# Kernel optimization log

Measured on AMD Instinct MI355X. Metric: run time of the kernel, lower is better.

Reference implementation:

```python
import jax, jax.numpy as jnp
import numpy as np

N = 100000
E = 1600000
D_IN = 64
D_HID = 64
D_OUT = 64


def setup_inputs() -> dict:
    key = jax.random.key(0)
    ks = jax.random.split(key, 12)
    x = jax.random.normal(ks[0], (N, D_IN), dtype=jnp.float32)
    edge_index = jax.random.randint(ks[1], (2, E), 0, N, dtype=jnp.int64)
    s1 = 1.0 / np.sqrt(D_IN)
    s2 = 1.0 / np.sqrt(D_HID)
    return {
        "x": x,
        "edge_index": edge_index,
        "W1l": jax.random.uniform(ks[2], (D_HID, D_IN), jnp.float32, -s1, s1),
        "b1l": jax.random.uniform(ks[3], (D_HID,), jnp.float32, -s1, s1),
        "W1r": jax.random.uniform(ks[4], (D_HID, D_IN), jnp.float32, -s1, s1),
        "W2l": jax.random.uniform(ks[5], (D_HID, D_HID), jnp.float32, -s2, s2),
        "b2l": jax.random.uniform(ks[6], (D_HID,), jnp.float32, -s2, s2),
        "W2r": jax.random.uniform(ks[7], (D_HID, D_HID), jnp.float32, -s2, s2),
        "Wout": jax.random.uniform(ks[8], (D_OUT, D_HID), jnp.float32, -s2, s2),
        "bout": jax.random.uniform(ks[9], (D_OUT,), jnp.float32, -s2, s2),
        "drop": 0,
    }


def _sage_conv(x, src, dst, Wl, bl, Wr, n_nodes):
    # PyG SAGEConv, aggr='mean': out = lin_l(mean_j x_j) + lin_r(x_i)
    msg = x[src]                                            # [E, d] gather
    agg = jax.ops.segment_sum(msg, dst, num_segments=n_nodes)
    deg = jax.ops.segment_sum(jnp.ones((src.shape[0],), x.dtype), dst,
                              num_segments=n_nodes)
    mean = agg / jnp.maximum(deg, 1.0)[:, None]             # empty neighborhoods -> 0
    return mean @ Wl.T + bl + x @ Wr.T


def reference(x, edge_index, W1l, b1l, W1r, W2l, b2l, W2r, Wout, bout, drop):
    src, dst = edge_index[0], edge_index[1]
    n = x.shape[0]
    # dropout is identity in eval mode (training=False); drop unused
    h = jax.nn.relu(_sage_conv(x, src, dst, W1l, b1l, W1r, n))
    h = jax.nn.relu(_sage_conv(h, src, dst, W2l, b2l, W2r, n))
    logits = h @ Wout.T + bout
    return jax.nn.log_softmax(logits, axis=1)
```

## Files before the change

kernel.cpp:

```cpp
#include <hip/hip_runtime.h>


#define TB 256
#define TBA 1024
#define NBINA 256
#define XFB 512
#define CAPC 32
#define NBPAD 1024

typedef __attribute__((ext_vector_type(8))) short bf16x8;
typedef __attribute__((ext_vector_type(4))) float f32x4;
typedef __attribute__((ext_vector_type(2))) float f32x2;

__device__ __forceinline__ unsigned short bf16c(float f) {
  union { float f; unsigned u; } v; v.f = f;
  unsigned r = (v.u + 0x7FFFu + ((v.u >> 16) & 1u)) >> 16;
  return (unsigned short)r;
}

__device__ __forceinline__ bf16x8 ld_bf8(const float* p) {
  float4 a = *(const float4*)p;
  float4 b = *(const float4*)(p + 4);
  bf16x8 r;
  r[0] = bf16c(a.x); r[1] = bf16c(a.y); r[2] = bf16c(a.z); r[3] = bf16c(a.w);
  r[4] = bf16c(b.x); r[5] = bf16c(b.y); r[6] = bf16c(b.z); r[7] = bf16c(b.w);
  return r;
}

__device__ __forceinline__ float bflo(unsigned u) { return __uint_as_float(u << 16); }
__device__ __forceinline__ float bfhi(unsigned u) { return __uint_as_float(u & 0xFFFF0000u); }
__device__ __forceinline__ unsigned bfpk(float lo, float hi) {
  return (unsigned)bf16c(lo) | ((unsigned)bf16c(hi) << 16);
}

__global__ __launch_bounds__(1024) void k_binA(
    const int* __restrict__ ei, int E,
    int* __restrict__ cellcnt, unsigned int* __restrict__ bucketData, int NB) {
  __shared__ int lcnt[NBPAD];
  __shared__ int s_nz;
  if (threadIdx.x == 0) s_nz = 0;
  for (int i = threadIdx.x; i < NBPAD; i += TBA) lcnt[i] = 0;
  __syncthreads();
  int nz = 0;
  for (int i = threadIdx.x; i < 2048; i += TBA) nz |= ei[2 * i + 1];
  if (nz) atomicOr(&s_nz, 1);
  __syncthreads();
  bool m64 = (s_nz == 0);
  int bb = blockIdx.x;

  long long e0 = (long long)E * bb / NBINA;
  long long e1 = (long long)E * (bb + 1) / NBINA;
  for (long long e = e0 + threadIdx.x; e < e1; e += TBA) {
    int src, dst;
    if (m64) {
      src = ((const int2*)ei)[e].x;
      dst = ((const int2*)ei)[(long long)E + e].x;
    } else {
      src = ei[e];
      dst = ei[(long long)E + e];
    }
    int b = dst >> 7;
    int pos = atomicAdd(&lcnt[b], 1);
    if (pos < CAPC)
      bucketData[((size_t)b * NBINA + bb) * CAPC + pos] =
          ((unsigned)(dst & 127) << 24) | (unsigned)src;
  }
  __syncthreads();
  for (int b = threadIdx.x; b < NB; b += TBA) cellcnt[bb * NBPAD + b] = lcnt[b];
}

__global__ __launch_bounds__(256) void k_binB_xf(
    const unsigned int* __restrict__ bucketData, const int* __restrict__ cellcnt,
    int* __restrict__ colp, int* __restrict__ cnt, int NB,
    const float* __restrict__ xin, const float* __restrict__ Wl,
    const float* __restrict__ Wr, const float* __restrict__ bl,
    unsigned short* __restrict__ y, unsigned short* __restrict__ zout, int n) {
  if (blockIdx.x < (unsigned)NB) {
    __shared__ unsigned int slice[128 * 64];
    __shared__ int lcnt[128];
    int b = blockIdx.x;
    for (int i = threadIdx.x; i < 128; i += TB) lcnt[i] = 0;
    __syncthreads();
    int c = cellcnt[threadIdx.x * NBPAD + b];
    if (c > CAPC) c = CAPC;
    const unsigned int* cell = bucketData + ((size_t)b * NBINA + threadIdx.x) * CAPC;
    for (int k = 0; k < c; ++k) {
      unsigned int rec = cell[k];
      int dl = rec >> 24;
      int pos = atomicAdd(&lcnt[dl], 1);
      if (pos < 64) slice[(dl << 6) + pos] = rec & 0xFFFFFFu;
    }
    __syncthreads();
    size_t obase = (size_t)b * (128 * 64);
    for (int i = threadIdx.x * 4; i < 128 * 64; i += TB * 4) {
      *(uint4*)(colp + obase + i) = *(const uint4*)(slice + i);
    }
    int node0 = b << 7;
    for (int i = threadIdx.x; i < 128; i += TB) cnt[node0 + i] = lcnt[i];
    return;
  }

  int lane = threadIdx.x & 63;
  int quad = lane >> 4, m = lane & 15;
  int w0 = ((blockIdx.x - NB) * TB + threadIdx.x) >> 6;
  int nw = (XFB * TB) >> 6;

  bf16x8 bfrag[8][2];
  float bias[4];
#pragma unroll
  for (int t = 0; t < 8; ++t) {
    const float* W = (t < 4) ? Wl : Wr;
    int row = (t & 3) * 16 + m;
#pragma unroll
    for (int s = 0; s < 2; ++s)
      bfrag[t][s] = ld_bf8(W + row * 64 + s * 32 + quad * 8);
  }
#pragma unroll
  for (int t = 0; t < 4; ++t) bias[t] = bl[t * 16 + m];

  int nT = (n + 15) >> 4;
  for (int tile = w0; tile < nT; tile += nw) {
    int node0 = tile << 4;
    int mrow = node0 + m;
    if (mrow >= n) mrow = n - 1;
    const float* xr = xin + (size_t)mrow * 64;
    bf16x8 a0 = ld_bf8(xr + quad * 8);
    bf16x8 a1 = ld_bf8(xr + 32 + quad * 8);

    f32x4 acc[8];
#pragma unroll
    for (int t = 0; t < 8; ++t) {
      f32x4 z4 = {0.f, 0.f, 0.f, 0.f};
      z4 = __builtin_amdgcn_mfma_f32_16x16x32_bf16(a0, bfrag[t][0], z4, 0, 0, 0);
      acc[t] = __builtin_amdgcn_mfma_f32_16x16x32_bf16(a1, bfrag[t][1], z4, 0, 0, 0);
    }

#pragma unroll
    for (int r = 0; r < 4; ++r) {
      int node = node0 + quad * 4 + r;
      if (node >= n) break;
      size_t rb = (size_t)node * 64 + m;
#pragma unroll
      for (int t = 0; t < 4; ++t) y[rb + t * 16] = bf16c(acc[t][r]);
#pragma unroll
      for (int t = 0; t < 4; ++t) zout[rb + t * 16] = bf16c(acc[t + 4][r] + bias[t]);
    }
  }
}

__global__ __launch_bounds__(256) void k_xform_b16(
    const unsigned short* zin, const float* __restrict__ Wl,
    const float* __restrict__ Wr, const float* __restrict__ bl,
    unsigned short* __restrict__ y, unsigned short* zout, int n) {
  int lane = threadIdx.x & 63;
  int quad = lane >> 4, m = lane & 15;
  int w0 = (blockIdx.x * blockDim.x + threadIdx.x) >> 6;
  int nw = (gridDim.x * blockDim.x) >> 6;

  bf16x8 bfrag[8][2];
  float bias[4];
#pragma unroll
  for (int t = 0; t < 8; ++t) {
    const float* W = (t < 4) ? Wl : Wr;
    int row = (t & 3) * 16 + m;
#pragma unroll
    for (int s = 0; s < 2; ++s)
      bfrag[t][s] = ld_bf8(W + row * 64 + s * 32 + quad * 8);
  }
#pragma unroll
  for (int t = 0; t < 4; ++t) bias[t] = bl[t * 16 + m];

  int nT = (n + 15) >> 4;
  for (int tile = w0; tile < nT; tile += nw) {
    int node0 = tile << 4;
    int mrow = node0 + m;
    if (mrow >= n) mrow = n - 1;
    const unsigned short* xr = zin + (size_t)mrow * 64;
    bf16x8 a0 = *(const bf16x8*)(xr + quad * 8);
    bf16x8 a1 = *(const bf16x8*)(xr + 32 + quad * 8);

    f32x4 acc[8];
#pragma unroll
    for (int t = 0; t < 8; ++t) {
      f32x4 z4 = {0.f, 0.f, 0.f, 0.f};
      z4 = __builtin_amdgcn_mfma_f32_16x16x32_bf16(a0, bfrag[t][0], z4, 0, 0, 0);
      acc[t] = __builtin_amdgcn_mfma_f32_16x16x32_bf16(a1, bfrag[t][1], z4, 0, 0, 0);
    }

#pragma unroll
    for (int r = 0; r < 4; ++r) {
      int node = node0 + quad * 4 + r;
      if (node >= n) break;
      size_t rb = (size_t)node * 64 + m;
#pragma unroll
      for (int t = 0; t < 4; ++t) y[rb + t * 16] = bf16c(acc[t][r]);
#pragma unroll
      for (int t = 0; t < 4; ++t) zout[rb + t * 16] = bf16c(acc[t + 4][r] + bias[t]);
    }
  }
}

__global__ __launch_bounds__(256) void k_aggr(
    const unsigned short* __restrict__ yb, const int* __restrict__ cnt,
    const int* __restrict__ colp, unsigned short* zio, int n) {
  const unsigned int* y = (const unsigned int*)yb;
  int lane = threadIdx.x & 63;
  int wv = (blockIdx.x * blockDim.x + threadIdx.x) >> 6;
  int g16 = lane & 48;
  int lig = lane & 15;
  int sub = lig >> 3;
  int fo = (lig & 7) * 4;

  int node = (wv << 2) + (g16 >> 4);
  bool act = node < n;
  int cn = act ? node : 0;
  int deg = cnt[cn];
  int jcap = deg < 64 ? deg : 64;
  size_t crow = (size_t)cn << 6;
  int cidxA = colp[crow + lig];
  int cidxB = colp[crow + 16 + lig];

  int wmax = jcap;
  wmax = max(wmax, __shfl_xor(wmax, 16, 64));
  wmax = max(wmax, __shfl_xor(wmax, 32, 64));

  f32x2 acc[4];
#pragma unroll
  for (int k = 0; k < 4; ++k) acc[k] = (f32x2){0.f, 0.f};

#define ACCUM(U)                                             \
  do {                                                       \
    acc[0] += (f32x2){bflo((U).x), bfhi((U).x)};             \
    acc[1] += (f32x2){bflo((U).y), bfhi((U).y)};             \
    acc[2] += (f32x2){bflo((U).z), bfhi((U).z)};             \
    acc[3] += (f32x2){bflo((U).w), bfhi((U).w)};             \
  } while (0)

#pragma unroll
  for (int s = 0; s < 16; s += 2) {
    int slot = s + sub;
    int c = __shfl(cidxA, g16 | slot, 64);
    if (slot < jcap) {
      uint4 v = *(const uint4*)(y + ((size_t)c << 5) + fo);
      ACCUM(v);
    }
  }
  if (wmax > 16) {
#pragma unroll
    for (int s = 0; s < 16; s += 2) {
      int slot = s + sub;
      int c = __shfl(cidxB, g16 | slot, 64);
      if (slot + 16 < jcap) {
        uint4 v = *(const uint4*)(y + ((size_t)c << 5) + fo);
        ACCUM(v);
      }
    }
  }
  if (wmax > 32) {
    int cidxC = colp[crow + 32 + lig];
    int cidxD = colp[crow + 48 + lig];
    {
      int lim = (wmax < 48 ? wmax : 48) - 32;
      for (int s = 0; s < lim; s += 2) {
        int slot = s + sub;
        int c = __shfl(cidxC, g16 | slot, 64);
        if (slot + 32 < jcap) {
          uint4 v = *(const uint4*)(y + ((size_t)c << 5) + fo);
          ACCUM(v);
        }
      }
    }
    if (wmax > 48) {
      int lim = wmax - 48;
      for (int s = 0; s < lim; s += 2) {
        int slot = s + sub;
        int c = __shfl(cidxD, g16 | slot, 64);
        if (slot + 48 < jcap) {
          uint4 v = *(const uint4*)(y + ((size_t)c << 5) + fo);
          ACCUM(v);
        }
      }
    }
  }
#undef ACCUM

#pragma unroll
  for (int k = 0; k < 4; ++k) {
    acc[k].x += __shfl_xor(acc[k].x, 8, 64);
    acc[k].y += __shfl_xor(acc[k].y, 8, 64);
  }

  if (act && sub == 0) {
    float inv = (deg > 0) ? 1.0f / (float)deg : 0.f;
    unsigned int* zp = (unsigned int*)(zio + ((size_t)node << 6)) + fo;
    uint4 zv = *(uint4*)zp;
    zv.x = bfpk(fmaxf(fmaf(acc[0].x, inv, bflo(zv.x)), 0.f),
                fmaxf(fmaf(acc[0].y, inv, bfhi(zv.x)), 0.f));
    zv.y = bfpk(fmaxf(fmaf(acc[1].x, inv, bflo(zv.y)), 0.f),
                fmaxf(fmaf(acc[1].y, inv, bfhi(zv.y)), 0.f));
    zv.z = bfpk(fmaxf(fmaf(acc[2].x, inv, bflo(zv.z)), 0.f),
                fmaxf(fmaf(acc[2].y, inv, bfhi(zv.z)), 0.f));
    zv.w = bfpk(fmaxf(fmaf(acc[3].x, inv, bflo(zv.w)), 0.f),
                fmaxf(fmaf(acc[3].y, inv, bfhi(zv.w)), 0.f));
    *(uint4*)zp = zv;
  }
}

__global__ __launch_bounds__(256) void k_out(
    const unsigned short* __restrict__ h, const float* __restrict__ Wo,
    const float* __restrict__ bo, float* __restrict__ out, int n) {
  int lane = threadIdx.x & 63;
  int quad = lane >> 4, m = lane & 15;
  int w0 = (blockIdx.x * blockDim.x + threadIdx.x) >> 6;
  int nw = (gridDim.x * blockDim.x) >> 6;

  bf16x8 bfrag[4][2];
  float bias[4];
#pragma unroll
  for (int t = 0; t < 4; ++t) {
    int row = t * 16 + m;
#pragma unroll
    for (int s = 0; s < 2; ++s)
      bfrag[t][s] = ld_bf8(Wo + row * 64 + s * 32 + quad * 8);
    bias[t] = bo[t * 16 + m];
  }

  int nT = (n + 15) >> 4;
  for (int tile = w0; tile < nT; tile += nw) {
    int node0 = tile << 4;
    int mrow = node0 + m;
    if (mrow >= n) mrow = n - 1;
    const unsigned short* xr = h + (size_t)mrow * 64;
    bf16x8 a0 = *(const bf16x8*)(xr + quad * 8);
    bf16x8 a1 = *(const bf16x8*)(xr + 32 + quad * 8);

    f32x4 acc[4];
#pragma unroll
    for (int t = 0; t < 4; ++t) {
      f32x4 z4 = {0.f, 0.f, 0.f, 0.f};
      z4 = __builtin_amdgcn_mfma_f32_16x16x32_bf16(a0, bfrag[t][0], z4, 0, 0, 0);
      acc[t] = __builtin_amdgcn_mfma_f32_16x16x32_bf16(a1, bfrag[t][1], z4, 0, 0, 0);
    }

#pragma unroll
    for (int r = 0; r < 4; ++r) {
      int node = node0 + quad * 4 + r;
      if (node >= n) break;
      float l0 = acc[0][r] + bias[0];
      float l1 = acc[1][r] + bias[1];
      float l2 = acc[2][r] + bias[2];
      float l3 = acc[3][r] + bias[3];
      float mx = fmaxf(fmaxf(l0, l1), fmaxf(l2, l3));
#pragma unroll
      for (int off = 1; off <= 8; off <<= 1) mx = fmaxf(mx, __shfl_xor(mx, off, 64));
      float s = expf(l0 - mx) + expf(l1 - mx) + expf(l2 - mx) + expf(l3 - mx);
#pragma unroll
      for (int off = 1; off <= 8; off <<= 1) s += __shfl_xor(s, off, 64);
      float ls = logf(s);
      size_t rb = (size_t)node * 64 + m;
      out[rb + 0]  = l0 - mx - ls;
      out[rb + 16] = l1 - mx - ls;
      out[rb + 32] = l2 - mx - ls;
      out[rb + 48] = l3 - mx - ls;
    }
  }
}

extern "C" void kernel_launch(void* const* d_in, const int* in_sizes, int n_in,
                              void* d_out, int out_size, void* d_ws, size_t ws_size,
                              hipStream_t stream) {
  const float* x    = (const float*)d_in[0];
  const int*   ei   = (const int*)d_in[1];
  const float* W1l  = (const float*)d_in[2];
  const float* b1l  = (const float*)d_in[3];
  const float* W1r  = (const float*)d_in[4];
  const float* W2l  = (const float*)d_in[5];
  const float* b2l  = (const float*)d_in[6];
  const float* W2r  = (const float*)d_in[7];
  const float* Wout = (const float*)d_in[8];
  const float* bout = (const float*)d_in[9];
  int N = in_sizes[0] / 64;
  int E = in_sizes[1] / 2;
  int NB = (N + 127) >> 7;

  char* p = (char*)d_ws;
  auto carve = [&](size_t bytes) {
    char* r = p;
    p += (bytes + 255) & ~(size_t)255;
    return r;
  };
  int* cellcnt       = (int*)carve((size_t)NBINA * NBPAD * 4);
  int* cnt           = (int*)carve((size_t)NB * 128 * 4);
  int* colp          = (int*)carve((size_t)NB * 128 * 64 * 4);
  unsigned short* y  = (unsigned short*)carve((size_t)N * 64 * 2);
  unsigned short* z  = (unsigned short*)carve((size_t)N * 64 * 2);
  unsigned int* bucketData = (unsigned int*)carve((size_t)NB * NBINA * CAPC * 4);

  int aggr_blocks = (N + 15) / 16;
  k_binA<<<NBINA, TBA, 0, stream>>>(ei, E, cellcnt, bucketData, NB);
  k_binB_xf<<<NB + XFB, TB, 0, stream>>>(bucketData, cellcnt, colp, cnt, NB,
                                         x, W1l, W1r, b1l, y, z, N);
  k_aggr<<<aggr_blocks, TB, 0, stream>>>(y, cnt, colp, z, N);
  k_xform_b16<<<XFB, TB, 0, stream>>>(z, W2l, W2r, b2l, y, z, N);
  k_aggr<<<aggr_blocks, TB, 0, stream>>>(y, cnt, colp, z, N);
  k_out<<<XFB, TB, 0, stream>>>(z, Wout, bout, (float*)d_out, N);
}
```

Before: 242.2 us.

## Split fused bin/transform kernel and pad LDS slice with vectorized cell reads

Splits the combined binning-B and first-layer transform kernel into two separate launches, so the bin blocks no longer carry the transform's register footprint and the transform blocks no longer reserve the 32KB slice in LDS. The bin kernel now reads bucket cells as uint4 with an unrolled loop and pads slice rows to 68 words to reduce LDS bank conflicts on scatter. In exchange it adds a kernel launch and loses the overlap between the two phases that the fused kernel allowed.

```diff
diff --git a/kernel.cpp b/kernel.cpp
--- a/kernel.cpp
+++ b/kernel.cpp
@@ -7,6 +7,7 @@
 #define XFB 512
 #define CAPC 32
 #define NBPAD 1024
+#define SP 68
 
 typedef __attribute__((ext_vector_type(8))) short bf16x8;
 typedef __attribute__((ext_vector_type(4))) float f32x4;
@@ -69,41 +70,51 @@
   for (int b = threadIdx.x; b < NB; b += TBA) cellcnt[bb * NBPAD + b] = lcnt[b];
 }
 
-__global__ __launch_bounds__(256) void k_binB_xf(
+__global__ __launch_bounds__(256) void k_binB(
     const unsigned int* __restrict__ bucketData, const int* __restrict__ cellcnt,
-    int* __restrict__ colp, int* __restrict__ cnt, int NB,
+    int* __restrict__ colp, int* __restrict__ cnt) {
+  __shared__ unsigned int slice[128 * SP];
+  __shared__ int lcnt[128];
+  int b = blockIdx.x;
+  for (int i = threadIdx.x; i < 128; i += TB) lcnt[i] = 0;
+  __syncthreads();
+  int c = cellcnt[threadIdx.x * NBPAD + b];
+  if (c > CAPC) c = CAPC;
+  const uint4* cell4 =
+      (const uint4*)(bucketData + ((size_t)b * NBINA + threadIdx.x) * CAPC);
+#pragma unroll
+  for (int k4 = 0; k4 < CAPC / 4; ++k4) {
+    if (k4 * 4 >= c) break;
+    uint4 r4 = cell4[k4];
+#pragma unroll
+    for (int j = 0; j < 4; ++j) {
+      int k = k4 * 4 + j;
+      if (k < c) {
+        unsigned rec = (&r4.x)[j];
+        int dl = rec >> 24;
+        int pos = atomicAdd(&lcnt[dl], 1);
+        if (pos < 64) slice[dl * SP + pos] = rec & 0xFFFFFFu;
+      }
+    }
+  }
+  __syncthreads();
+  size_t obase = (size_t)b * (128 * 64);
+  for (int i = threadIdx.x * 4; i < 128 * 64; i += TB * 4) {
+    int node = i >> 6, j = i & 63;
+    *(uint4*)(colp + obase + i) = *(const uint4*)(slice + node * SP + j);
+  }
+  int node0 = b << 7;
+  for (int i = threadIdx.x; i < 128; i += TB) cnt[node0 + i] = lcnt[i];
+}
+
+__global__ __launch_bounds__(256) void k_xform_f32(
     const float* __restrict__ xin, const float* __restrict__ Wl,
     const float* __restrict__ Wr, const float* __restrict__ bl,
     unsigned short* __restrict__ y, unsigned short* __restrict__ zout, int n) {
-  if (blockIdx.x < (unsigned)NB) {
-    __shared__ unsigned int slice[128 * 64];
-    __shared__ int lcnt[128];
-    int b = blockIdx.x;
-    for (int i = threadIdx.x; i < 128; i += TB) lcnt[i] = 0;
-    __syncthreads();
-    int c = cellcnt[threadIdx.x * NBPAD + b];
-    if (c > CAPC) c = CAPC;
-    const unsigned int* cell = bucketData + ((size_t)b * NBINA + threadIdx.x) * CAPC;
-    for (int k = 0; k < c; ++k) {
-      unsigned int rec = cell[k];
-      int dl = rec >> 24;
-      int pos = atomicAdd(&lcnt[dl], 1);
-      if (pos < 64) slice[(dl << 6) + pos] = rec & 0xFFFFFFu;
-    }
-    __syncthreads();
-    size_t obase = (size_t)b * (128 * 64);
-    for (int i = threadIdx.x * 4; i < 128 * 64; i += TB * 4) {
-      *(uint4*)(colp + obase + i) = *(const uint4*)(slice + i);
-    }
-    int node0 = b << 7;
-    for (int i = threadIdx.x; i < 128; i += TB) cnt[node0 + i] = lcnt[i];
-    return;
-  }
-
   int lane = threadIdx.x & 63;
   int quad = lane >> 4, m = lane & 15;
-  int w0 = ((blockIdx.x - NB) * TB + threadIdx.x) >> 6;
-  int nw = (XFB * TB) >> 6;
+  int w0 = (blockIdx.x * blockDim.x + threadIdx.x) >> 6;
+  int nw = (gridDim.x * blockDim.x) >> 6;
 
   bf16x8 bfrag[8][2];
   float bias[4];
@@ -398,8 +409,8 @@
 
   int aggr_blocks = (N + 15) / 16;
   k_binA<<<NBINA, TBA, 0, stream>>>(ei, E, cellcnt, bucketData, NB);
-  k_binB_xf<<<NB + XFB, TB, 0, stream>>>(bucketData, cellcnt, colp, cnt, NB,
-                                         x, W1l, W1r, b1l, y, z, N);
+  k_binB<<<NB, TB, 0, stream>>>(bucketData, cellcnt, colp, cnt);
+  k_xform_f32<<<XFB, TB, 0, stream>>>(x, W1l, W1r, b1l, y, z, N);
   k_aggr<<<aggr_blocks, TB, 0, stream>>>(y, cnt, colp, z, N);
   k_xform_b16<<<XFB, TB, 0, stream>>>(z, W2l, W2r, b2l, y, z, N);
   k_aggr<<<aggr_blocks, TB, 0, stream>>>(y, cnt, colp, z, N);
```

New measurement: 236.3 us. 1.02x faster.
